# Optimization experiments

Measured on AMD Instinct MI355X. Metric: run time of the kernel, lower is better.

## Reference

```python
import jax, jax.numpy as jnp
import numpy as np

R = 8            # receptive_field (hardcoded r=8 in GridProcessing call)
MARGIN = 0.6     # TripletLoss(margin=0.6)
EPS = 1e-8       # F.cosine_similarity eps


def _mine_cords(B, FH, FW):
    """Replicates GridProcessing._prepare for an identity flow field
    G[b, y, x] = ((x + 0.5) / W, (y + 0.5) / H):
    at every cell center, G_xmin = x, G_xmax = x + 1, both inside bounds, and
    [x // r, (x + 1) // r + 1) = {ix}, so the positive window collapses to the
    cell itself -> anchor_cord == positive_cord == (b, ix, iy) for every cell.
    (clip(0, 31) is benign since FH = FW = 32.)
    Negative cords from _prepare are discarded by forward(), so not produced."""
    bs, ys, xs = np.meshgrid(np.arange(B), np.arange(FH), np.arange(FW), indexing='ij')
    idx = np.stack([bs, xs, ys], axis=-1).reshape(-1, 3).astype(np.int32)  # rows: (b, x, y)
    return idx, idx.copy()


def setup_inputs() -> dict:
    key = jax.random.key(0)
    B, C, FH, FW = 16, 1024, 32, 32
    k1, k2 = jax.random.split(key)
    sketch = jax.random.normal(k1, (B, C, FH, FW), dtype=jnp.float32)
    ref = jax.random.normal(k2, (B, C, FH, FW), dtype=jnp.float32)
    a_idx, p_idx = _mine_cords(B, FH, FW)
    return {
        'sketch_query_vectors': sketch,
        'ref_key_vectors': ref,
        'anchor_idx': jnp.asarray(a_idx),
        'positive_idx': jnp.asarray(p_idx),
    }


def reference(sketch_query_vectors, ref_key_vectors, anchor_idx, positive_idx):
    B, C, FH, FW = sketch_query_vectors.shape
    HW = FH * FW
    N = anchor_idx.shape[0]
    na = N // B  # anchor rows are ordered by batch index, na anchors per image

    ax = anchor_idx[:, 1].reshape(B, na)
    ay = anchor_idx[:, 2].reshape(B, na)
    # anchor = sketch[b, :, y, x]  -> (B, na, C)
    a = sketch_query_vectors[jnp.arange(B)[:, None], :, ay, ax]

    # ref_fs.view(c, h*w).permute(1, 0): row-major flatten, flat id = y*W + x
    ref_flat = ref_key_vectors.reshape(B, C, HW).transpose(0, 2, 1)  # (B, HW, C)

    # cosine similarity of every anchor vs every ref position (per batch)
    dots = jnp.einsum('bnc,bmc->bnm', a, ref_flat)          # (B, na, HW)
    a_n = jnp.linalg.norm(a, axis=-1)                        # (B, na)
    r_n = jnp.linalg.norm(ref_flat, axis=-1)                 # (B, HW)
    sim = dots / jnp.maximum(a_n[:, :, None] * r_n[:, None, :], EPS)

    # get_negative_ids: argsort(dist)[:3] -> 3 LOWEST cosine positions;
    # loss uses sum of the 3 anchor-negative cosines (broadcasted cosine sum)
    neg_sum = -jnp.sum(jax.lax.top_k(-sim, 3)[0], axis=-1)   # (B, na)

    # cos(anchor, positive) is just sim at the positive's flat position
    pos_flat = (positive_idx[:, 2] * FW + positive_idx[:, 1]).reshape(B, na)
    cos_ap = jnp.take_along_axis(sim, pos_flat[:, :, None], axis=2)[..., 0]

    # (1 - cos_ap) - (1 - neg_sum) + margin, relu, mean over the single triplet
    losses = jax.nn.relu(neg_sum - cos_ap + MARGIN)          # (B, na)
    return jnp.sum(losses) / (1e-6 + N)
```

## Files before the change

kernel.cpp:

```cpp
#include <hip/hip_runtime.h>
#include <hip/hip_bf16.h>
#include <stdint.h>

#define BATCH 16
#define CDIM  1024
#define FWID  32
#define HW    1024
#define NA    1024
#define NTOT  (BATCH*NA)
#define NCHUNK 16
#define MARGIN 0.6f

typedef __bf16 bf16x8 __attribute__((ext_vector_type(8)));
typedef float  f32x4  __attribute__((ext_vector_type(4)));
typedef unsigned short us4 __attribute__((ext_vector_type(4)));
typedef unsigned short us8 __attribute__((ext_vector_type(8)));
typedef float  f4     __attribute__((ext_vector_type(4)));

template<int OFF>
__device__ __forceinline__ us4 tr_read(uint32_t addr){
  us4 r;
  asm volatile("ds_read_b64_tr_b16 %0, %1 offset:%2" : "=v"(r) : "v"(addr), "n"(OFF));
  return r;
}

__device__ __forceinline__ void gload16(const unsigned short* g, unsigned short* l){
  __builtin_amdgcn_global_load_lds((const __attribute__((address_space(1))) void*)g,
                                   (__attribute__((address_space(3))) void*)l, 16, 0, 0);
}

union FragU  { us4 h[2]; bf16x8 v; };
union FragU8 { us8 u;    bf16x8 v; };

__device__ __forceinline__ void ins3(float& a, float& b, float& c, float v){
  if (v < c){
    c = v;
    if (c < b){ float t=b; b=c; c=t;
      if (b < a){ t=a; a=b; b=t; }
    }
  }
}

#define MFMA __builtin_amdgcn_mfma_f32_16x16x32_bf16

__global__ __launch_bounds__(512)
void convert_transpose4(const float* __restrict__ S, const float* __restrict__ R,
                        unsigned short* __restrict__ tS, unsigned short* __restrict__ tR,
                        float* __restrict__ snorm){
  __shared__ unsigned short tile[64*1032];
  __shared__ float nsq[64][33];

  const int blk = blockIdx.x;
  const int e   = blk >> 8;
  const int b   = (blk >> 4) & 15;
  const int hwT = blk & 15;
  const float* src = (e ? R : S) + (size_t)b*CDIM*HW;
  unsigned short* dst = (e ? tR : tS) + (size_t)b*HW*CDIM;

  const int t  = threadIdx.x;
  const int li = t & 15;
  const int gi = t >> 4;
  const int hwb = hwT*64 + li*4;

  float sq0=0.f, sq1=0.f, sq2=0.f, sq3=0.f;
  #pragma unroll
  for (int it = 0; it < 4; ++it){
    const int cb = it*256 + gi*8;
    f4 col[8];
    #pragma unroll
    for (int i = 0; i < 8; ++i)
      col[i] = *(const f4*)&src[(size_t)(cb + i)*HW + hwb];
    #pragma unroll
    for (int j = 0; j < 4; ++j){
      us8 pk;
      float sq = 0.f;
      #pragma unroll
      for (int i = 0; i < 8; ++i){
        __hip_bfloat16 h = __float2bfloat16(col[i][j]);
        pk[i] = __builtin_bit_cast(unsigned short, h);
        const float g = __bfloat162float(h);
        sq = fmaf(g, g, sq);
      }
      *(us8*)&tile[(li*4 + j)*1032 + cb] = pk;
      if (j==0) sq0+=sq; else if (j==1) sq1+=sq; else if (j==2) sq2+=sq; else sq3+=sq;
    }
  }
  nsq[li*4+0][gi] = sq0;
  nsq[li*4+1][gi] = sq1;
  nsq[li*4+2][gi] = sq2;
  nsq[li*4+3][gi] = sq3;
  __syncthreads();

  const int w = t >> 6, l = t & 63;
  #pragma unroll
  for (int rr = 0; rr < 8; ++rr){
    const int row = w*8 + rr;
    const us8 v0 = *(const us8*)&tile[row*1032 + l*8];
    const us8 v1 = *(const us8*)&tile[row*1032 + 512 + l*8];
    unsigned short* drow = dst + (size_t)(hwT*64 + row)*CDIM;
    *(us8*)(drow + l*8)       = v0;
    *(us8*)(drow + 512 + l*8) = v1;
  }

  if (t < 64){
    float a = 0.f;
    #pragma unroll
    for (int g2 = 0; g2 < 32; ++g2) a += nsq[t][g2];
    snorm[(size_t)(e*16 + b)*HW + hwT*64 + t] = sqrtf(a);
  }
}

__global__ __launch_bounds__(512, 2)
void fused_gemm_top3_v9(const unsigned short* __restrict__ tS,
                        const unsigned short* __restrict__ tR,
                        const float* __restrict__ snorm,
                        const int*   __restrict__ anchor,
                        const int*   __restrict__ posidx,
                        float* __restrict__ wtop,
                        float* __restrict__ wpos)
{
  __shared__ unsigned short stage[65536];
  __shared__ int   p_lds[256], q_lds[256];
  __shared__ float nAs[256], nBs[256];

  const int t = threadIdx.x;
  const uint32_t bid = blockIdx.x;
  const uint32_t L = (bid & 7u)*32u + (bid >> 3);
  const int b  = L >> 4;
  const int ni = (L >> 2) & 3;
  const int mi = L & 3;

  const unsigned short* SbT = tS + (size_t)b*HW*CDIM;
  const unsigned short* RbT = tR + (size_t)b*HW*CDIM;

  if (t < 256){
    const int n_g = ni*256 + t;
    const int* ap = anchor + (size_t)(b*NA + n_g)*3;
    const int* pp = posidx + (size_t)(b*NA + n_g)*3;
    const int pv = ap[2]*FWID + ap[1];
    p_lds[t] = pv;
    q_lds[t] = pp[2]*FWID + pp[1];
    nAs[t] = 1.0f / snorm[(size_t)b*HW + pv];
  } else {
    nBs[t-256] = 1.0f / snorm[(size_t)(BATCH + b)*HW + mi*256 + (t-256)];
  }
  __syncthreads();

  const int l  = t & 63;
  const int w  = t >> 6;
  const int wr = w >> 2, wc = w & 3;

  const int gkc = (l&7) ^ ((l>>3)&7);
  const unsigned short* gA[4];
  const unsigned short* gB[4];
  #pragma unroll
  for (int i = 0; i < 4; ++i){
    const int row = w*32 + i*8 + (l>>3);
    gA[i] = SbT + (size_t)p_lds[row]*CDIM + gkc*8;
    gB[i] = RbT + (size_t)(mi*256 + row)*CDIM + gkc*8;
  }
  unsigned short* lA = &stage[w*2048];
  unsigned short* lB = &stage[32768 + w*2048];

  const int fb0 = (l&15)*64 + (((l>>4)    ) ^ (l&7))*8;
  const int fb1 = (l&15)*64 + (((l>>4) + 4) ^ (l&7))*8;
  const int abase = wr*8192;
  const int bbase = 32768 + wc*4096;

  f32x4 acc[8][4];
  #pragma unroll
  for (int i=0;i<8;i++){
    #pragma unroll
    for (int j=0;j<4;j++){ f32x4 z = {0.f,0.f,0.f,0.f}; acc[i][j] = z; }
  }

  auto stage8 = [&](int bo, int kt){
    const int ko = kt*64;
    #pragma unroll
    for (int i = 0; i < 4; ++i){
      gload16(gA[i] + ko, lA + bo + i*512);
      gload16(gB[i] + ko, lB + bo + i*512);
    }
  };

  auto half = [&](int bo, int fbh){
    FragU8 Bf[4], Af[8];
    #pragma unroll
    for (int fb=0; fb<4; ++fb) Bf[fb].u = *(const us8*)&stage[bbase + bo + fb*1024 + fbh];
    #pragma unroll
    for (int fa=0; fa<8; ++fa) Af[fa].u = *(const us8*)&stage[abase + bo + fa*1024 + fbh];
    __builtin_amdgcn_s_setprio(1);
    #pragma unroll
    for (int fa=0; fa<8; ++fa){
      #pragma unroll
      for (int fb=0; fb<4; ++fb)
        acc[fa][fb] = MFMA(Af[fa].v, Bf[fb].v, acc[fa][fb], 0,0,0);
    }
    __builtin_amdgcn_s_setprio(0);
  };

  stage8(0, 0);
  int bo = 0;
  for (int kt = 0; kt < 16; ++kt){
    asm volatile("s_waitcnt vmcnt(0)" ::: "memory");
    __builtin_amdgcn_s_barrier();
    __builtin_amdgcn_sched_barrier(0);
    if (kt < 15) stage8(bo ^ 16384, kt+1);
    half(bo, fb0);
    half(bo, fb1);
    bo ^= 16384;
  }

  __syncthreads();
  float* tls = (float*)&stage[0] + (size_t)w*1152;

  float rinv[4];
  #pragma unroll
  for (int fb=0; fb<4; ++fb) rinv[fb] = nBs[wc*64 + fb*16 + (l&15)];

  #pragma unroll
  for (int fa=0; fa<8; ++fa){
    #pragma unroll
    for (int r=0; r<4; ++r){
      const int rg    = (l>>4)*4 + r;
      const int row_l = wr*128 + fa*16 + rg;
      const float ain = nAs[row_l];
      const float v0 = acc[fa][0][r] * ain * rinv[0];
      const float v1 = acc[fa][1][r] * ain * rinv[1];
      const float v2 = acc[fa][2][r] * ain * rinv[2];
      const float v3 = acc[fa][3][r] * ain * rinv[3];

      const int n_g = ni*256 + row_l;
      const int q   = q_lds[row_l];
      const int ql  = q - (mi*256 + wc*64);
      if (ql >= 0 && ql < 64 && (ql & 15) == (l & 15)){
        const int sel = ql >> 4;
        const float pv = sel==0 ? v0 : sel==1 ? v1 : sel==2 ? v2 : v3;
        wpos[b*NA + n_g] = pv;
      }

      float x=1e30f, y=1e30f, z=1e30f;
      ins3(x,y,z,v0); ins3(x,y,z,v1); ins3(x,y,z,v2); ins3(x,y,z,v3);
      f4 tr = {x, y, z, 0.f};
      *(f4*)(tls + (rg*17 + (l&15))*4) = tr;
    }
    asm volatile("s_waitcnt lgkmcnt(0)" ::: "memory");
    __builtin_amdgcn_sched_barrier(0);

    {
      const int rr = l >> 2;
      const float* rbp = tls + (rr*17 + (l&3)*4)*4;
      const f4 t0 = *(const f4*)(rbp);
      const f4 t1 = *(const f4*)(rbp + 4);
      const f4 t2 = *(const f4*)(rbp + 8);
      const f4 t3 = *(const f4*)(rbp + 12);
      float x = t0[0], y = t0[1], z = t0[2];
      ins3(x,y,z,t1[0]); ins3(x,y,z,t1[1]); ins3(x,y,z,t1[2]);
      ins3(x,y,z,t2[0]); ins3(x,y,z,t2[1]); ins3(x,y,z,t2[2]);
      ins3(x,y,z,t3[0]); ins3(x,y,z,t3[1]); ins3(x,y,z,t3[2]);
      #pragma unroll
      for (int m=1; m<4; m<<=1){
        const float ox = __shfl_xor(x, m);
        const float oy = __shfl_xor(y, m);
        const float oz = __shfl_xor(z, m);
        ins3(x,y,z,ox); ins3(x,y,z,oy); ins3(x,y,z,oz);
      }
      if ((l & 3) == 0){
        const int n_g = ni*256 + wr*128 + fa*16 + rr;
        float* dst = wtop + ((size_t)(b*NA + n_g)*NCHUNK + (mi*4 + wc))*3;
        dst[0]=x; dst[1]=y; dst[2]=z;
      }
    }
    asm volatile("s_waitcnt lgkmcnt(0)" ::: "memory");
    __builtin_amdgcn_sched_barrier(0);
  }
}

__global__ __launch_bounds__(256)
void fused_gemm_top3_v1(const float* __restrict__ sketch,
                        const float* __restrict__ refk,
                        const int*   __restrict__ anchor,
                        const int*   __restrict__ posidx,
                        float* __restrict__ wtop,
                        float* __restrict__ wpos)
{
  __shared__ union {
    unsigned short stage[16384];
    struct { float nA[16][128]; float nB[16][128]; } nrm;
  } sh;
  __shared__ int   p_lds[128];
  __shared__ float nA2[128], nB2[128];

  const int t = threadIdx.x;
  const uint32_t bid = blockIdx.x;
  const uint32_t L = (bid & 7u)*128u + (bid >> 3);
  const int b  = L >> 6;
  const int ni = (L >> 3) & 7;
  const int mi = L & 7;

  const float* Sb = sketch + (size_t)b*CDIM*HW;
  const float* Rb = refk   + (size_t)b*CDIM*HW;

  if (t < 128){
    const int n_g = ni*128 + t;
    const int* ap = anchor + (size_t)(b*NA + n_g)*3;
    p_lds[t] = ap[2]*FWID + ap[1];
  }
  __syncthreads();
  const int p0 = p_lds[0];
  int okf = 1;
  if (t < 128) okf = (p_lds[t] == p0 + t);
  const int contig = __syncthreads_and(okf);

  const int colg = (t & 15)*8;
  const int rowg = t >> 4;
  const int mbase = mi*128;

  const int l  = t & 63;
  const int w  = t >> 6;
  const int wr = w >> 1, wc = w & 1;
  const uint32_t sh_base = (uint32_t)(uintptr_t)&sh.stage[0];
  const uint32_t laneA = ((uint32_t)(l>>4))*2048u + (uint32_t)wr*512u + (uint32_t)(l&15)*8u;
  const uint32_t laneB = ((uint32_t)(l>>4))*2048u + (uint32_t)wc*512u + (uint32_t)(l&15)*8u;
  const int off0 = ((rowg>>2)*8 + (colg>>4))*64 + (rowg&3)*16 + (colg&15);

  f32x4 acc[4][4];
  #pragma unroll
  for (int i=0;i<4;i++){
    #pragma unroll
    for (int j=0;j<4;j++){ f32x4 z = {0.f,0.f,0.f,0.f}; acc[i][j] = z; }
  }

  float sqA[8] = {0,0,0,0,0,0,0,0};
  float sqB[8] = {0,0,0,0,0,0,0,0};
  f4 ra[4], rb[4];

  auto load_tile = [&](int kt){
    const int c0 = kt*32 + rowg;
    const float* SA = Sb + (size_t)c0*HW;
    const float* RB = Rb + (size_t)c0*HW + mbase + colg;
    if (contig){
      const float* pA = SA + p0 + colg;
      ra[0] = *(const f4*)(pA);
      ra[1] = *(const f4*)(pA + 4);
      ra[2] = *(const f4*)(pA + 16*HW);
      ra[3] = *(const f4*)(pA + 16*HW + 4);
    } else {
      float* raf = (float*)ra;
      #pragma unroll
      for (int i=0;i<8;i++){
        const int pc = p_lds[colg + i];
        raf[i]   = SA[pc];
        raf[8+i] = SA[16*HW + pc];
      }
    }
    rb[0] = *(const f4*)(RB);
    rb[1] = *(const f4*)(RB + 4);
    rb[2] = *(const f4*)(RB + 16*HW);
    rb[3] = *(const f4*)(RB + 16*HW + 4);
  };

  auto cvt_store = [&](int buf){
    const float* raf = (const float*)ra;
    const float* rbf = (const float*)rb;
    us8 pk;
    #pragma unroll
    for (int i=0;i<8;i++){
      __hip_bfloat16 h = __float2bfloat16(raf[i]);
      pk[i] = __builtin_bit_cast(unsigned short, h);
      const float g = __bfloat162float(h);
      sqA[i] = fmaf(g, g, sqA[i]);
    }
    *(us8*)&sh.stage[buf*4096 + off0] = pk;
    #pragma unroll
    for (int i=0;i<8;i++){
      __hip_bfloat16 h = __float2bfloat16(raf[8+i]);
      pk[i] = __builtin_bit_cast(unsigned short, h);
      const float g = __bfloat162float(h);
      sqA[i] = fmaf(g, g, sqA[i]);
    }
    *(us8*)&sh.stage[buf*4096 + off0 + 2048] = pk;
    #pragma unroll
    for (int i=0;i<8;i++){
      __hip_bfloat16 h = __float2bfloat16(rbf[i]);
      pk[i] = __builtin_bit_cast(unsigned short, h);
      const float g = __bfloat162float(h);
      sqB[i] = fmaf(g, g, sqB[i]);
    }
    *(us8*)&sh.stage[8192 + buf*4096 + off0] = pk;
    #pragma unroll
    for (int i=0;i<8;i++){
      __hip_bfloat16 h = __float2bfloat16(rbf[8+i]);
      pk[i] = __builtin_bit_cast(unsigned short, h);
      const float g = __bfloat162float(h);
      sqB[i] = fmaf(g, g, sqB[i]);
    }
    *(us8*)&sh.stage[8192 + buf*4096 + off0 + 2048] = pk;
  };

  auto compute = [&](int buf){
    const uint32_t aaddr = sh_base + (uint32_t)buf*8192u + laneA;
    const uint32_t baddr = sh_base + 16384u + (uint32_t)buf*8192u + laneB;
    FragU A0,A1,A2,A3,B0,B1,B2,B3;
    A0.h[0]=tr_read<0>(aaddr);    A0.h[1]=tr_read<1024>(aaddr);
    A1.h[0]=tr_read<128>(aaddr);  A1.h[1]=tr_read<1152>(aaddr);
    A2.h[0]=tr_read<256>(aaddr);  A2.h[1]=tr_read<1280>(aaddr);
    A3.h[0]=tr_read<384>(aaddr);  A3.h[1]=tr_read<1408>(aaddr);
    B0.h[0]=tr_read<0>(baddr);    B0.h[1]=tr_read<1024>(baddr);
    B1.h[0]=tr_read<128>(baddr);  B1.h[1]=tr_read<1152>(baddr);
    B2.h[0]=tr_read<256>(baddr);  B2.h[1]=tr_read<1280>(baddr);
    B3.h[0]=tr_read<384>(baddr);  B3.h[1]=tr_read<1408>(baddr);
    asm volatile("s_waitcnt lgkmcnt(0)" ::: "memory");
    __builtin_amdgcn_sched_barrier(0);
    acc[0][0]=MFMA(A0.v,B0.v,acc[0][0],0,0,0);
    acc[0][1]=MFMA(A0.v,B1.v,acc[0][1],0,0,0);
    acc[0][2]=MFMA(A0.v,B2.v,acc[0][2],0,0,0);
    acc[0][3]=MFMA(A0.v,B3.v,acc[0][3],0,0,0);
    acc[1][0]=MFMA(A1.v,B0.v,acc[1][0],0,0,0);
    acc[1][1]=MFMA(A1.v,B1.v,acc[1][1],0,0,0);
    acc[1][2]=MFMA(A1.v,B2.v,acc[1][2],0,0,0);
    acc[1][3]=MFMA(A1.v,B3.v,acc[1][3],0,0,0);
    acc[2][0]=MFMA(A2.v,B0.v,acc[2][0],0,0,0);
    acc[2][1]=MFMA(A2.v,B1.v,acc[2][1],0,0,0);
    acc[2][2]=MFMA(A2.v,B2.v,acc[2][2],0,0,0);
    acc[2][3]=MFMA(A2.v,B3.v,acc[2][3],0,0,0);
    acc[3][0]=MFMA(A3.v,B0.v,acc[3][0],0,0,0);
    acc[3][1]=MFMA(A3.v,B1.v,acc[3][1],0,0,0);
    acc[3][2]=MFMA(A3.v,B2.v,acc[3][2],0,0,0);
    acc[3][3]=MFMA(A3.v,B3.v,acc[3][3],0,0,0);
  };

  load_tile(0);
  cvt_store(0);
  __syncthreads();
  int buf = 0;
  for (int kt = 0; kt < 32; ++kt){
    if (kt < 31) load_tile(kt+1);
    compute(buf);
    if (kt < 31) cvt_store(buf^1);
    __syncthreads();
    buf ^= 1;
  }

  #pragma unroll
  for (int i=0;i<8;i++) sh.nrm.nA[rowg][colg+i] = sqA[i];
  #pragma unroll
  for (int i=0;i<8;i++) sh.nrm.nB[rowg][colg+i] = sqB[i];
  __syncthreads();
  if (t < 128){
    float s = 0.f;
    #pragma unroll
    for (int r=0;r<16;r++) s += sh.nrm.nA[r][t];
    nA2[t] = s;
  } else {
    const int c2 = t - 128;
    float s = 0.f;
    #pragma unroll
    for (int r=0;r<16;r++) s += sh.nrm.nB[r][c2];
    nB2[c2] = s;
  }
  __syncthreads();

  float rncol[4];
  #pragma unroll
  for (int nf=0;nf<4;nf++) rncol[nf] = sqrtf(nB2[wc*64 + nf*16 + (l&15)]);

  #pragma unroll
  for (int mf=0; mf<4; ++mf){
    #pragma unroll
    for (int r=0; r<4; ++r){
      const int row_l = wr*64 + mf*16 + (l>>4)*4 + r;
      const int n_g   = ni*128 + row_l;
      const float an  = sqrtf(nA2[row_l]);
      const float v0 = acc[mf][0][r] / fmaxf(an*rncol[0], 1e-8f);
      const float v1 = acc[mf][1][r] / fmaxf(an*rncol[1], 1e-8f);
      const float v2 = acc[mf][2][r] / fmaxf(an*rncol[2], 1e-8f);
      const float v3 = acc[mf][3][r] / fmaxf(an*rncol[3], 1e-8f);

      const int* pp = posidx + (size_t)(b*NA + n_g)*3;
      const int q  = pp[2]*FWID + pp[1];
      const int ql = q - (mbase + wc*64);
      if (ql >= 0 && ql < 64 && (ql & 15) == (l & 15)){
        const int sel = ql >> 4;
        const float pv = sel==0 ? v0 : sel==1 ? v1 : sel==2 ? v2 : v3;
        wpos[b*NA + n_g] = pv;
      }

      float x=1e30f, y=1e30f, z=1e30f;
      ins3(x,y,z,v0); ins3(x,y,z,v1); ins3(x,y,z,v2); ins3(x,y,z,v3);
      #pragma unroll
      for (int m=1; m<16; m<<=1){
        const float ox = __shfl_xor(x, m);
        const float oy = __shfl_xor(y, m);
        const float oz = __shfl_xor(z, m);
        ins3(x,y,z,ox); ins3(x,y,z,oy); ins3(x,y,z,oz);
      }
      if ((l & 15) == 0){
        float* dst = wtop + ((size_t)(b*NA + n_g)*NCHUNK + (mi*2 + wc))*3;
        dst[0]=x; dst[1]=y; dst[2]=z;
      }
    }
  }
}

__global__ __launch_bounds__(256)
void merge_top3(const float* __restrict__ wtop, const float* __restrict__ wpos,
                float* __restrict__ partial){
  __shared__ float red[256];
  const int id = blockIdx.x*256 + threadIdx.x;
  const float* src = wtop + (size_t)id*(NCHUNK*3);
  float x=1e30f, y=1e30f, z=1e30f;
  #pragma unroll
  for (int i=0;i<NCHUNK*3;i++) ins3(x,y,z, src[i]);
  const float loss = fmaxf((x+y+z) - wpos[id] + MARGIN, 0.0f);
  red[threadIdx.x] = loss;
  __syncthreads();
  for (int s=128; s>0; s>>=1){
    if (threadIdx.x < s) red[threadIdx.x] += red[threadIdx.x+s];
    __syncthreads();
  }
  if (threadIdx.x == 0) partial[blockIdx.x] = red[0];
}

__global__ void final_sum(const float* __restrict__ partial, float* __restrict__ out){
  float v = partial[threadIdx.x];
  #pragma unroll
  for (int off=32; off>0; off>>=1) v += __shfl_down(v, off);
  if (threadIdx.x == 0) out[0] = v / (1e-6f + (float)NTOT);
}

extern "C" void kernel_launch(void* const* d_in, const int* in_sizes, int n_in,
                              void* d_out, int out_size, void* d_ws, size_t ws_size,
                              hipStream_t stream){
  const float* sketch = (const float*)d_in[0];
  const float* refk   = (const float*)d_in[1];
  const int*   anchor = (const int*)d_in[2];
  const int*   posidx = (const int*)d_in[3];
  float* out = (float*)d_out;

  float* wtop    = (float*)d_ws;
  float* wpos    = wtop + (size_t)NTOT*NCHUNK*3;
  float* partial = wpos + NTOT;
  unsigned short* tS = (unsigned short*)(partial + 256);
  unsigned short* tR = tS + (size_t)BATCH*HW*CDIM;
  float* snorm = (float*)(tR + (size_t)BATCH*HW*CDIM);
  const size_t need = (size_t)((char*)(snorm + 32*1024) - (char*)d_ws);

  if (ws_size >= need){
    convert_transpose4<<<dim3(512), dim3(512), 0, stream>>>(sketch, refk, tS, tR, snorm);
    fused_gemm_top3_v9<<<dim3(256), dim3(512), 0, stream>>>(tS, tR, snorm, anchor, posidx, wtop, wpos);
  } else {
    fused_gemm_top3_v1<<<dim3(1024), dim3(256), 0, stream>>>(sketch, refk, anchor, posidx, wtop, wpos);
  }
  merge_top3<<<dim3(64), dim3(256), 0, stream>>>(wtop, wpos, partial);
  final_sum<<<dim3(1), dim3(64), 0, stream>>>(partial, out);
}
```

Before: 95.16 us.

## Tile transpose by channel blocks, pad transposed rows, split norm reduction

The convert/transpose kernel now tiles over 64-channel blocks instead of 64-spatial blocks. Each row of source floats is read contiguously, transposed through a padded LDS tile, and written as 128-byte segments into a transposed buffer with a padded row pitch of 1088. Per-channel-block partial squared norms go to a workspace and are reduced by a new small kernel. The padded pitch is meant to spread GEMM row loads across memory channels. The cost is an extra kernel launch, a larger workspace, and scalar 2-byte LDS stores during the transpose.

```diff
diff --git a/kernel.cpp b/kernel.cpp
--- a/kernel.cpp
+++ b/kernel.cpp
@@ -10,6 +10,7 @@
 #define NTOT  (BATCH*NA)
 #define NCHUNK 16
 #define MARGIN 0.6f
+#define TPITCH 1088
 
 typedef __bf16 bf16x8 __attribute__((ext_vector_type(8)));
 typedef float  f32x4  __attribute__((ext_vector_type(4)));
@@ -44,80 +45,85 @@
 #define MFMA __builtin_amdgcn_mfma_f32_16x16x32_bf16
 
 __global__ __launch_bounds__(512)
-void convert_transpose4(const float* __restrict__ S, const float* __restrict__ R,
+void convert_transpose5(const float* __restrict__ S, const float* __restrict__ R,
                         unsigned short* __restrict__ tS, unsigned short* __restrict__ tR,
-                        float* __restrict__ snorm){
-  __shared__ unsigned short tile[64*1032];
-  __shared__ float nsq[64][33];
+                        float* __restrict__ pnorm){
+  __shared__ unsigned short tileT[1024*68];
 
   const int blk = blockIdx.x;
   const int e   = blk >> 8;
   const int b   = (blk >> 4) & 15;
-  const int hwT = blk & 15;
+  const int cT  = blk & 15;
   const float* src = (e ? R : S) + (size_t)b*CDIM*HW;
-  unsigned short* dst = (e ? tR : tS) + (size_t)b*HW*CDIM;
-
+  unsigned short* dst = (e ? tR : tS) + (size_t)b*HW*TPITCH;
+
+  const int t = threadIdx.x;
+  const int w = t >> 6, l = t & 63;
+  const int c0 = cT*64 + w*8;
+
+  #pragma unroll
+  for (int rr = 0; rr < 8; ++rr){
+    const float* srow = src + (size_t)(c0 + rr)*HW;
+    #pragma unroll
+    for (int i = 0; i < 4; ++i){
+      const int hwb = i*256 + l*4;
+      const f4 v = *(const f4*)&srow[hwb];
+      #pragma unroll
+      for (int s = 0; s < 4; ++s){
+        __hip_bfloat16 h = __float2bfloat16(v[s]);
+        tileT[(hwb + s)*68 + w*8 + rr] = __builtin_bit_cast(unsigned short, h);
+      }
+    }
+  }
+  __syncthreads();
+
+  const int r8 = t >> 3;
+  const int sg = t & 7;
+  #pragma unroll
+  for (int k = 0; k < 16; ++k){
+    const int h = r8 + 64*k;
+    const unsigned short* row = &tileT[h*68 + sg*8];
+    us8 pk;
+    #pragma unroll
+    for (int j = 0; j < 8; ++j) pk[j] = row[j];
+    *(us8*)&dst[(size_t)h*TPITCH + cT*64 + sg*8] = pk;
+    float sq = 0.f;
+    #pragma unroll
+    for (int j = 0; j < 8; ++j){
+      const float g = __bfloat162float(__builtin_bit_cast(__hip_bfloat16, pk[j]));
+      sq = fmaf(g, g, sq);
+    }
+    sq += __shfl_xor(sq, 1);
+    sq += __shfl_xor(sq, 2);
+    sq += __shfl_xor(sq, 4);
+    if (sg == 0)
+      pnorm[((size_t)(e*16 + b)*16 + cT)*HW + h] = sq;
+  }
+}
+
+__global__ __launch_bounds__(256)
+void norm_reduce16(const float* __restrict__ pnorm, float* __restrict__ snorm){
+  const int eb = blockIdx.x;
   const int t  = threadIdx.x;
-  const int li = t & 15;
-  const int gi = t >> 4;
-  const int hwb = hwT*64 + li*4;
-
-  float sq0=0.f, sq1=0.f, sq2=0.f, sq3=0.f;
-  #pragma unroll
-  for (int it = 0; it < 4; ++it){
-    const int cb = it*256 + gi*8;
-    f4 col[8];
-    #pragma unroll
-    for (int i = 0; i < 8; ++i)
-      col[i] = *(const f4*)&src[(size_t)(cb + i)*HW + hwb];
-    #pragma unroll
-    for (int j = 0; j < 4; ++j){
-      us8 pk;
-      float sq = 0.f;
-      #pragma unroll
-      for (int i = 0; i < 8; ++i){
-        __hip_bfloat16 h = __float2bfloat16(col[i][j]);
-        pk[i] = __builtin_bit_cast(unsigned short, h);
-        const float g = __bfloat162float(h);
-        sq = fmaf(g, g, sq);
-      }
-      *(us8*)&tile[(li*4 + j)*1032 + cb] = pk;
-      if (j==0) sq0+=sq; else if (j==1) sq1+=sq; else if (j==2) sq2+=sq; else sq3+=sq;
-    }
-  }
-  nsq[li*4+0][gi] = sq0;
-  nsq[li*4+1][gi] = sq1;
-  nsq[li*4+2][gi] = sq2;
-  nsq[li*4+3][gi] = sq3;
-  __syncthreads();
-
-  const int w = t >> 6, l = t & 63;
-  #pragma unroll
-  for (int rr = 0; rr < 8; ++rr){
-    const int row = w*8 + rr;
-    const us8 v0 = *(const us8*)&tile[row*1032 + l*8];
-    const us8 v1 = *(const us8*)&tile[row*1032 + 512 + l*8];
-    unsigned short* drow = dst + (size_t)(hwT*64 + row)*CDIM;
-    *(us8*)(drow + l*8)       = v0;
-    *(us8*)(drow + 512 + l*8) = v1;
-  }
-
-  if (t < 64){
+  #pragma unroll
+  for (int r = 0; r < 4; ++r){
+    const int hw = r*256 + t;
     float a = 0.f;
     #pragma unroll
-    for (int g2 = 0; g2 < 32; ++g2) a += nsq[t][g2];
-    snorm[(size_t)(e*16 + b)*HW + hwT*64 + t] = sqrtf(a);
+    for (int ct = 0; ct < 16; ++ct)
+      a += pnorm[((size_t)eb*16 + ct)*HW + hw];
+    snorm[(size_t)eb*HW + hw] = sqrtf(a);
   }
 }
 
 __global__ __launch_bounds__(512, 2)
-void fused_gemm_top3_v9(const unsigned short* __restrict__ tS,
-                        const unsigned short* __restrict__ tR,
-                        const float* __restrict__ snorm,
-                        const int*   __restrict__ anchor,
-                        const int*   __restrict__ posidx,
-                        float* __restrict__ wtop,
-                        float* __restrict__ wpos)
+void fused_gemm_top3_v9p(const unsigned short* __restrict__ tS,
+                         const unsigned short* __restrict__ tR,
+                         const float* __restrict__ snorm,
+                         const int*   __restrict__ anchor,
+                         const int*   __restrict__ posidx,
+                         float* __restrict__ wtop,
+                         float* __restrict__ wpos)
 {
   __shared__ unsigned short stage[65536];
   __shared__ int   p_lds[256], q_lds[256];
@@ -130,8 +136,8 @@
   const int ni = (L >> 2) & 3;
   const int mi = L & 3;
 
-  const unsigned short* SbT = tS + (size_t)b*HW*CDIM;
-  const unsigned short* RbT = tR + (size_t)b*HW*CDIM;
+  const unsigned short* SbT = tS + (size_t)b*HW*TPITCH;
+  const unsigned short* RbT = tR + (size_t)b*HW*TPITCH;
 
   if (t < 256){
     const int n_g = ni*256 + t;
@@ -156,8 +162,8 @@
   #pragma unroll
   for (int i = 0; i < 4; ++i){
     const int row = w*32 + i*8 + (l>>3);
-    gA[i] = SbT + (size_t)p_lds[row]*CDIM + gkc*8;
-    gB[i] = RbT + (size_t)(mi*256 + row)*CDIM + gkc*8;
+    gA[i] = SbT + (size_t)p_lds[row]*TPITCH + gkc*8;
+    gB[i] = RbT + (size_t)(mi*256 + row)*TPITCH + gkc*8;
   }
   unsigned short* lA = &stage[w*2048];
   unsigned short* lB = &stage[32768 + w*2048];
@@ -542,13 +548,15 @@
   float* wpos    = wtop + (size_t)NTOT*NCHUNK*3;
   float* partial = wpos + NTOT;
   unsigned short* tS = (unsigned short*)(partial + 256);
-  unsigned short* tR = tS + (size_t)BATCH*HW*CDIM;
-  float* snorm = (float*)(tR + (size_t)BATCH*HW*CDIM);
+  unsigned short* tR = tS + (size_t)BATCH*HW*TPITCH;
+  float* pnorm = (float*)(tR + (size_t)BATCH*HW*TPITCH);
+  float* snorm = pnorm + (size_t)32*16*1024;
   const size_t need = (size_t)((char*)(snorm + 32*1024) - (char*)d_ws);
 
   if (ws_size >= need){
-    convert_transpose4<<<dim3(512), dim3(512), 0, stream>>>(sketch, refk, tS, tR, snorm);
-    fused_gemm_top3_v9<<<dim3(256), dim3(512), 0, stream>>>(tS, tR, snorm, anchor, posidx, wtop, wpos);
+    convert_transpose5<<<dim3(512), dim3(512), 0, stream>>>(sketch, refk, tS, tR, pnorm);
+    norm_reduce16<<<dim3(32), dim3(256), 0, stream>>>(pnorm, snorm);
+    fused_gemm_top3_v9p<<<dim3(256), dim3(512), 0, stream>>>(tS, tR, snorm, anchor, posidx, wtop, wpos);
   } else {
     fused_gemm_top3_v1<<<dim3(1024), dim3(256), 0, stream>>>(sketch, refk, anchor, posidx, wtop, wpos);
   }
```

Result: slower. 98.34 us (+3.4%).
